# Kernel tuning notes

Hardware: AMD Instinct MI355X
Metric: run time of the kernel (lower is better)

The kernel has to match this reference:

```python
import jax, jax.numpy as jnp
import numpy as np

SEM_DIM = 512
SEM_SIZE = 2048
N_LEVELS = 9           # acoustic FSQ levels
HALF = (N_LEVELS - 1) / 2.0
EPS = 1e-5


def setup_inputs() -> dict:
    key = jax.random.key(0)
    k1, k2, k3, k4, k5, k6 = jax.random.split(key, 6)
    B, T, ACO_DIM = 16, 4096, 32
    return {
        "x": jax.random.normal(k1, (B, SEM_DIM + ACO_DIM, T), dtype=jnp.float32),
        "embedding_sum": jax.random.normal(k2, (SEM_SIZE, SEM_DIM), dtype=jnp.float32),
        "cluster_usage": jax.random.uniform(k3, (SEM_SIZE,), dtype=jnp.float32),
        "noise": jax.random.uniform(k4, (B, ACO_DIM, T), dtype=jnp.float32),
        "probs_sem": jax.random.uniform(k5, (B,), dtype=jnp.float32),
        "probs_aco": jax.random.uniform(k6, (B,), dtype=jnp.float32),
    }


def reference(x, embedding_sum, cluster_usage, noise, probs_sem, probs_aco):
    sem_in = x[:, :SEM_DIM, :]          # [B, 512, T]
    aco_in = x[:, SEM_DIM:, :]          # [B, 32, T]
    B, D, T = sem_in.shape

    # ---- semantic VQ path (cdist + argmin + embedding lookup + STE) ----
    emb = embedding_sum / jnp.clip(cluster_usage, EPS, None)[:, None]  # [K, D]
    xf = sem_in.transpose(0, 2, 1).reshape(B * T, D)                   # (b t) d
    # squared euclidean distance (argmin identical to cdist p=2 argmin)
    d2 = (jnp.sum(xf * xf, axis=1, keepdims=True)
          - 2.0 * (xf @ emb.T)
          + jnp.sum(emb * emb, axis=1))                                # [BT, K]
    sem_codes = jnp.argmin(d2, axis=-1).reshape(B, 1, T)               # [B,1,T]
    sem_quant = emb[sem_codes[:, 0, :]].transpose(0, 2, 1)             # b d t
    sem_mask = (probs_sem < 0.5)[:, None, None]
    sem_ste = sem_in + jax.lax.stop_gradient(sem_quant - sem_in)
    sem_out = jnp.where(sem_mask, sem_ste, sem_in)

    # ---- acoustic FSQ path with 50/25/25 stochastic routing ----
    z_b = jnp.tanh(aco_in) * HALF
    z_q = z_b + jax.lax.stop_gradient(jnp.round(z_b) - z_b)            # round STE
    noise_s = (noise * 2.0 - 1.0) * (1.0 / N_LEVELS) * HALF            # U[-s, s]*half
    z_dither = jnp.clip(z_b + noise_s, -HALF, HALF)
    qm = (probs_aco < 0.5)[:, None, None]
    dm = ((probs_aco >= 0.5) & (probs_aco < 0.75))[:, None, None]
    z_out = jnp.where(qm, z_q, jnp.where(dm, z_dither, z_b))
    aco_codes = jnp.clip(jnp.round(z_out + HALF), 0, N_LEVELS - 1).astype(jnp.int32)
    z_norm = z_out / HALF

    quantized = jnp.concatenate([sem_out, z_norm], axis=1)             # [B,544,T]
    codes = jnp.concatenate([sem_codes.astype(jnp.int32), aco_codes], axis=1)
    return quantized, codes
```

## Files before the change

kernel.cpp:

```cpp
#include <hip/hip_runtime.h>
#include <math.h>

typedef _Float16 f16;
typedef _Float16 f16x8 __attribute__((ext_vector_type(8)));
typedef float f32x4 __attribute__((ext_vector_type(4)));

#define B_    16
#define T_    4096
#define SEM   512
#define ACO   32
#define XROWS 544
#define CODES 2048
#define EPSC  1e-5f
#define HALFC 4.0f
#define ECLAMP 60000.0f


__global__ void bias_kernel(const float* __restrict__ esum,
                            const float* __restrict__ usage,
                            float* __restrict__ bias) {
    int c = blockIdx.x;
    float u = fmaxf(usage[c], EPSC);
    float s = 0.f;
    for (int d = threadIdx.x; d < SEM; d += 64) {
        float v = esum[(size_t)c * SEM + d] / u;
        s += v * v;
    }
    for (int off = 32; off; off >>= 1) s += __shfl_down(s, off);
    if (threadIdx.x == 0) bias[c] = 0.5f * s;
}

__global__ void embT_kernel(const float* __restrict__ esum,
                            const float* __restrict__ usage,
                            float* __restrict__ embT) {
    __shared__ float tile[32][33];
    int c0 = blockIdx.x * 32;
    int d0 = blockIdx.y * 32;
    int col = threadIdx.x & 31, r = threadIdx.x >> 5;
    for (int i = r; i < 32; i += 8) {
        float u = fmaxf(usage[c0 + i], EPSC);
        tile[col][i] = esum[(size_t)(c0 + i) * SEM + d0 + col] / u;
    }
    __syncthreads();
    for (int i = r; i < 32; i += 8)
        embT[(size_t)(d0 + i) * CODES + c0 + col] = tile[i][col];
}

__global__ void esplit_kernel(const float* __restrict__ esum,
                              const float* __restrict__ usage,
                              f16* __restrict__ EhT, f16* __restrict__ ElT) {
    int c = blockIdx.x;
    float u = fmaxf(usage[c], EPSC);
    for (int d = threadIdx.x; d < SEM; d += 256) {
        float e = esum[(size_t)c * SEM + d] / u;
        e = fminf(fmaxf(e, -ECLAMP), ECLAMP);
        f16 h = (f16)e;
        EhT[(size_t)c * SEM + d] = h;
        ElT[(size_t)c * SEM + d] = (f16)(e - (float)h);
    }
}

#define MB 256
#define NQ 512
#define NC 128
#define BK 32
#define XPAD 258
__global__ __launch_bounds__(256, 2) void argmin_mfma(
        const float* __restrict__ x, const f16* __restrict__ EhT,
        const f16* __restrict__ ElT, const float* __restrict__ bias,
        float* __restrict__ pScore, int* __restrict__ pIdx) {
    __shared__ float Xs[BK * XPAD];
    __shared__ f16 Eh[NC * 32];
    __shared__ f16 El[NC * 32];

    int tid = threadIdx.x;
    int w   = tid >> 6;
    int l   = tid & 63;
    int q   = l >> 4;
    int r16 = l & 15;

    int m0      = blockIdx.x * MB;
    int quarter = blockIdx.y;
    int b  = m0 >> 12;
    int t0 = m0 & 4095;
    const float* xb = x + (size_t)b * XROWS * T_ + t0;

    float bestS[16];
    int   bestI[16];
#pragma unroll
    for (int i = 0; i < 16; i++) { bestS[i] = -3.4e38f; bestI[i] = 0; }

    for (int nc = 0; nc < 4; nc++) {
        int nbase = quarter * NQ + nc * NC;
        float bb[8];
#pragma unroll
        for (int ni = 0; ni < 8; ni++) bb[ni] = bias[nbase + ni * 16 + r16];

        f32x4 acc[4][8];
#pragma unroll
        for (int mi = 0; mi < 4; mi++)
#pragma unroll
            for (int ni = 0; ni < 8; ni++)
                acc[mi][ni] = (f32x4){0.f, 0.f, 0.f, 0.f};

        for (int k0 = 0; k0 < SEM; k0 += BK) {
            __syncthreads();
#pragma unroll
            for (int rr = 0; rr < 8; rr++) {
                int row = rr * 4 + w;
                float4 v = *(const float4*)(xb + (size_t)(k0 + row) * T_ + l * 4);
                *(float4*)&Xs[row * XPAD + l * 4] = v;
            }
#pragma unroll
            for (int pp = 0; pp < 2; pp++) {
                int row = (tid >> 2) + pp * 64;
                int kc  = (tid & 3) * 8;
                size_t g = (size_t)(nbase + row) * SEM + k0 + kc;
                *(float4*)&Eh[row * 32 + kc] = *(const float4*)(EhT + g);
                *(float4*)&El[row * 32 + kc] = *(const float4*)(ElT + g);
            }
            __syncthreads();

            f16x8 ah[4], al[4];
#pragma unroll
            for (int mi = 0; mi < 4; mi++) {
                int m = w * 64 + mi * 16 + r16;
#pragma unroll
                for (int j = 0; j < 8; j++) {
                    float v = Xs[(q * 8 + j) * XPAD + m];
                    f16 h = (f16)v;
                    ah[mi][j] = h;
                    al[mi][j] = (f16)(v - (float)h);
                }
            }
#pragma unroll
            for (int ni = 0; ni < 8; ni++) {
                f16x8 bh = *(const f16x8*)&Eh[(ni * 16 + r16) * 32 + q * 8];
                f16x8 bl = *(const f16x8*)&El[(ni * 16 + r16) * 32 + q * 8];
#pragma unroll
                for (int mi = 0; mi < 4; mi++) {
                    f32x4 a0 = acc[mi][ni];
                    a0 = __builtin_amdgcn_mfma_f32_16x16x32_f16(al[mi], bh, a0, 0, 0, 0);
                    a0 = __builtin_amdgcn_mfma_f32_16x16x32_f16(ah[mi], bl, a0, 0, 0, 0);
                    a0 = __builtin_amdgcn_mfma_f32_16x16x32_f16(ah[mi], bh, a0, 0, 0, 0);
                    acc[mi][ni] = a0;
                }
            }
        }
#pragma unroll
        for (int ni = 0; ni < 8; ni++) {
            int n = nbase + ni * 16 + r16;
#pragma unroll
            for (int mi = 0; mi < 4; mi++)
#pragma unroll
                for (int reg = 0; reg < 4; reg++) {
                    float s = acc[mi][ni][reg] - bb[ni];
                    int slot = mi * 4 + reg;
                    if (s > bestS[slot]) { bestS[slot] = s; bestI[slot] = n; }
                }
        }
    }

#pragma unroll
    for (int mask = 1; mask < 16; mask <<= 1) {
#pragma unroll
        for (int slot = 0; slot < 16; slot++) {
            float os = __shfl_xor(bestS[slot], mask);
            int   oi = __shfl_xor(bestI[slot], mask);
            if (os > bestS[slot] || (os == bestS[slot] && oi < bestI[slot])) {
                bestS[slot] = os; bestI[slot] = oi;
            }
        }
    }
    if (r16 == 0) {
#pragma unroll
        for (int mi = 0; mi < 4; mi++)
#pragma unroll
            for (int reg = 0; reg < 4; reg++) {
                int m = m0 + w * 64 + mi * 16 + q * 4 + reg;
                pScore[quarter * 65536 + m] = bestS[mi * 4 + reg];
                pIdx  [quarter * 65536 + m] = bestI[mi * 4 + reg];
            }
    }
}

__global__ void merge_kernel(const float* __restrict__ pScore,
                             const int* __restrict__ pIdx,
                             int* __restrict__ codesW,
                             float* __restrict__ codes_out) {
    int m = blockIdx.x * 256 + threadIdx.x;
    float bs = pScore[m]; int bi = pIdx[m];
    for (int qq = 1; qq < 4; qq++) {
        float s = pScore[qq * 65536 + m];
        int  ii = pIdx[qq * 65536 + m];
        if (s > bs || (s == bs && ii < bi)) { bs = s; bi = ii; }
    }
    codesW[m] = bi;
    int bb2 = m >> 12, t = m & 4095;
    codes_out[(size_t)bb2 * 33 * T_ + t] = (float)bi;
}

__global__ void finalize_kernel(const float* __restrict__ x,
                                const float* __restrict__ embT,
                                const int* __restrict__ codes_ws,
                                const float* __restrict__ noise,
                                const float* __restrict__ probs_sem,
                                const float* __restrict__ probs_aco,
                                float* __restrict__ out,
                                float* __restrict__ codes_out) {
    const size_t N0 = (size_t)B_ * SEM * T_;
    const size_t N1 = (size_t)B_ * ACO * T_;
    size_t idx = (size_t)blockIdx.x * 256 + threadIdx.x;
    if (idx < N0) {
        int t = (int)(idx & 4095);
        int d = (int)((idx >> 12) & 511);
        int b = (int)(idx >> 21);
        float v;
        if (probs_sem[b] < 0.5f) {
            int c = codes_ws[(b << 12) + t];
            v = embT[(size_t)d * CODES + c];
        } else {
            v = x[((size_t)(b * XROWS + d)) * T_ + t];
        }
        out[((size_t)(b * XROWS + d)) * T_ + t] = v;
    } else if (idx < N0 + N1) {
        size_t i2 = idx - N0;
        int t = (int)(i2 & 4095);
        int j = (int)((i2 >> 12) & 31);
        int b = (int)(i2 >> 17);
        float a  = x[((size_t)(b * XROWS + SEM + j)) * T_ + t];
        float zb = tanhf(a) * HALFC;
        float p  = probs_aco[b];
        float zo;
        if (p < 0.5f) {
            zo = rintf(zb);
        } else if (p < 0.75f) {
            float nz = noise[((size_t)(b * ACO + j)) * T_ + t];
            float ns = ((nz * 2.0f - 1.0f) * (float)(1.0 / 9.0)) * HALFC;
            zo = fminf(fmaxf(zb + ns, -HALFC), HALFC);
        } else {
            zo = zb;
        }
        float code = fminf(fmaxf(rintf(zo + HALFC), 0.f), 8.f);
        out[((size_t)(b * XROWS + SEM + j)) * T_ + t] = zo * 0.25f;
        codes_out[((size_t)(b * 33 + 1 + j)) * T_ + t] = code;
    }
}

extern "C" void kernel_launch(void* const* d_in, const int* in_sizes, int n_in,
                              void* d_out, int out_size, void* d_ws, size_t ws_size,
                              hipStream_t stream) {
    const float* x      = (const float*)d_in[0];
    const float* esum   = (const float*)d_in[1];
    const float* usage  = (const float*)d_in[2];
    const float* noise  = (const float*)d_in[3];
    const float* psem   = (const float*)d_in[4];
    const float* paco   = (const float*)d_in[5];
    float* out = (float*)d_out;

    float* wsf    = (float*)d_ws;
    float* embT   = wsf;
    float* bias   = wsf + 1048576;
    int*   codesW = (int*)(wsf + 1050624);
    f16*   EhT    = (f16*)(wsf + 1116160);
    f16*   ElT    = (f16*)(wsf + 1640448);
    float* pScore = wsf + 2164736;
    int*   pIdx   = (int*)(wsf + 2426880);

    const size_t QOFF = (size_t)B_ * XROWS * T_;
    float* codes_out = out + QOFF;

    bias_kernel<<<CODES, 64, 0, stream>>>(esum, usage, bias);
    embT_kernel<<<dim3(CODES / 32, SEM / 32), 256, 0, stream>>>(esum, usage, embT);
    esplit_kernel<<<CODES, 256, 0, stream>>>(esum, usage, EhT, ElT);
    argmin_mfma<<<dim3((B_ * T_) / MB, 4), 256, 0, stream>>>(x, EhT, ElT, bias,
                                                             pScore, pIdx);
    merge_kernel<<<(B_ * T_) / 256, 256, 0, stream>>>(pScore, pIdx, codesW, codes_out);
    const size_t NTOT = (size_t)B_ * SEM * T_ + (size_t)B_ * ACO * T_;
    finalize_kernel<<<(int)(NTOT / 256), 256, 0, stream>>>(x, embT, codesW, noise,
                                                           psem, paco, out, codes_out);
}
```

Measured before the change: 883.0 us.

## Pre-split X into transposed fp16 hi/lo buffers and load via global_load_lds

Adds a pre-pass that converts the semantic slice of x into transposed fp16 high/low parts, stored in the output buffer as scratch. The argmin MFMA kernel then loads ready-made fp16 tiles straight into LDS with global_load_lds, instead of loading fp32, staging it, and splitting it per k-step in every code quarter. This removes conversion work that was repeated four times and the strided LDS reads, at the cost of an extra pass over x and more global traffic for the split copies. It relies on the output buffer not being overwritten until finalize runs, which happens after argmin.

```diff
diff --git a/kernel.cpp b/kernel.cpp
--- a/kernel.cpp
+++ b/kernel.cpp
@@ -1,5 +1,6 @@
 #include <hip/hip_runtime.h>
 #include <math.h>
+#include <stdint.h>
 
 typedef _Float16 f16;
 typedef _Float16 f16x8 __attribute__((ext_vector_type(8)));
@@ -60,18 +61,56 @@
     }
 }
 
+__global__ void xsplit_kernel(const float* __restrict__ x,
+                              f16* __restrict__ XhT, f16* __restrict__ XlT) {
+    int m0 = blockIdx.x * 256;
+    int d0 = blockIdx.y * 32;
+    int b  = m0 >> 12;
+    int t  = (m0 & 4095) + (int)threadIdx.x;
+    const float* xp = x + ((size_t)b * XROWS + d0) * T_ + t;
+    int m = m0 + (int)threadIdx.x;
+
+    f16x8 hv[4], lv[4];
+#pragma unroll
+    for (int j = 0; j < 4; j++) {
+#pragma unroll
+        for (int e = 0; e < 8; e++) {
+            float v = xp[(size_t)(j * 8 + e) * T_];
+            f16 h = (f16)v;
+            hv[j][e] = h;
+            lv[j][e] = (f16)(v - (float)h);
+        }
+    }
+    f16* oh = XhT + (size_t)m * SEM + d0;
+    f16* ol = XlT + (size_t)m * SEM + d0;
+#pragma unroll
+    for (int j = 0; j < 4; j++) {
+        *(f16x8*)(oh + j * 8) = hv[j];
+        *(f16x8*)(ol + j * 8) = lv[j];
+    }
+}
+
 #define MB 256
 #define NQ 512
 #define NC 128
 #define BK 32
-#define XPAD 258
+
+__device__ __forceinline__ void gl_lds16(const f16* g, f16* l) {
+    __builtin_amdgcn_global_load_lds(
+        (const __attribute__((address_space(1))) unsigned int*)(g),
+        (__attribute__((address_space(3))) unsigned int*)(l),
+        16, 0, 0);
+}
+
 __global__ __launch_bounds__(256, 2) void argmin_mfma(
-        const float* __restrict__ x, const f16* __restrict__ EhT,
-        const f16* __restrict__ ElT, const float* __restrict__ bias,
+        const f16* __restrict__ XhT, const f16* __restrict__ XlT,
+        const f16* __restrict__ EhT, const f16* __restrict__ ElT,
+        const float* __restrict__ bias,
         float* __restrict__ pScore, int* __restrict__ pIdx) {
-    __shared__ float Xs[BK * XPAD];
-    __shared__ f16 Eh[NC * 32];
-    __shared__ f16 El[NC * 32];
+    __shared__ __align__(16) f16 Xh[MB * BK];
+    __shared__ __align__(16) f16 Xl[MB * BK];
+    __shared__ __align__(16) f16 Eh[NC * BK];
+    __shared__ __align__(16) f16 El[NC * BK];
 
     int tid = threadIdx.x;
     int w   = tid >> 6;
@@ -81,9 +120,9 @@
 
     int m0      = blockIdx.x * MB;
     int quarter = blockIdx.y;
-    int b  = m0 >> 12;
-    int t0 = m0 & 4095;
-    const float* xb = x + (size_t)b * XROWS * T_ + t0;
+
+    int aoff = (w * 64 + r16) * BK + q * 8;
+    int boff = r16 * BK + q * 8;
 
     float bestS[16];
     int   bestI[16];
@@ -106,37 +145,33 @@
         for (int k0 = 0; k0 < SEM; k0 += BK) {
             __syncthreads();
 #pragma unroll
-            for (int rr = 0; rr < 8; rr++) {
-                int row = rr * 4 + w;
-                float4 v = *(const float4*)(xb + (size_t)(k0 + row) * T_ + l * 4);
-                *(float4*)&Xs[row * XPAD + l * 4] = v;
-            }
-#pragma unroll
-            for (int pp = 0; pp < 2; pp++) {
-                int row = (tid >> 2) + pp * 64;
-                int kc  = (tid & 3) * 8;
-                size_t g = (size_t)(nbase + row) * SEM + k0 + kc;
-                *(float4*)&Eh[row * 32 + kc] = *(const float4*)(EhT + g);
-                *(float4*)&El[row * 32 + kc] = *(const float4*)(ElT + g);
+            for (int ii = 0; ii < 4; ii++) {
+                int off16 = ii * 256 + tid;
+                int mm = off16 >> 2, ch = off16 & 3;
+                int gsrc = (m0 + mm) * SEM + k0 + ch * 8;
+                gl_lds16(XhT + gsrc, Xh + off16 * 8);
+                gl_lds16(XlT + gsrc, Xl + off16 * 8);
+            }
+#pragma unroll
+            for (int ii = 0; ii < 2; ii++) {
+                int off16 = ii * 256 + tid;
+                int nn = off16 >> 2, ch = off16 & 3;
+                int gsrc = (nbase + nn) * SEM + k0 + ch * 8;
+                gl_lds16(EhT + gsrc, Eh + off16 * 8);
+                gl_lds16(ElT + gsrc, El + off16 * 8);
             }
             __syncthreads();
 
             f16x8 ah[4], al[4];
 #pragma unroll
             for (int mi = 0; mi < 4; mi++) {
-                int m = w * 64 + mi * 16 + r16;
-#pragma unroll
-                for (int j = 0; j < 8; j++) {
-                    float v = Xs[(q * 8 + j) * XPAD + m];
-                    f16 h = (f16)v;
-                    ah[mi][j] = h;
-                    al[mi][j] = (f16)(v - (float)h);
-                }
+                ah[mi] = *(const f16x8*)&Xh[aoff + mi * 16 * BK];
+                al[mi] = *(const f16x8*)&Xl[aoff + mi * 16 * BK];
             }
 #pragma unroll
             for (int ni = 0; ni < 8; ni++) {
-                f16x8 bh = *(const f16x8*)&Eh[(ni * 16 + r16) * 32 + q * 8];
-                f16x8 bl = *(const f16x8*)&El[(ni * 16 + r16) * 32 + q * 8];
+                f16x8 bh = *(const f16x8*)&Eh[boff + ni * 16 * BK];
+                f16x8 bl = *(const f16x8*)&El[boff + ni * 16 * BK];
 #pragma unroll
                 for (int mi = 0; mi < 4; mi++) {
                     f32x4 a0 = acc[mi][ni];
@@ -270,11 +305,15 @@
     const size_t QOFF = (size_t)B_ * XROWS * T_;
     float* codes_out = out + QOFF;
 
+    f16* XhT = (f16*)out;
+    f16* XlT = (f16*)(out + 16777216);
+
+    xsplit_kernel<<<dim3((B_ * T_) / 256, SEM / 32), 256, 0, stream>>>(x, XhT, XlT);
     bias_kernel<<<CODES, 64, 0, stream>>>(esum, usage, bias);
     embT_kernel<<<dim3(CODES / 32, SEM / 32), 256, 0, stream>>>(esum, usage, embT);
     esplit_kernel<<<CODES, 256, 0, stream>>>(esum, usage, EhT, ElT);
-    argmin_mfma<<<dim3((B_ * T_) / MB, 4), 256, 0, stream>>>(x, EhT, ElT, bias,
-                                                             pScore, pIdx);
+    argmin_mfma<<<dim3((B_ * T_) / MB, 4), 256, 0, stream>>>(XhT, XlT, EhT, ElT,
+                                                             bias, pScore, pIdx);
     merge_kernel<<<(B_ * T_) / 256, 256, 0, stream>>>(pScore, pIdx, codesW, codes_out);
     const size_t NTOT = (size_t)B_ * SEM * T_ + (size_t)B_ * ACO * T_;
     finalize_kernel<<<(int)(NTOT / 256), 256, 0, stream>>>(x, embT, codesW, noise,
```

Measured after the change: 828.8 us. 1.07x faster.
